# Kernel tuning notes

Measured on AMD Instinct MI355X. Metric: run time of the kernel, lower is better.

The kernel has to match this reference:

```python
import jax, jax.numpy as jnp
import numpy as np

N = 100000   # nodes
E = 1600000  # edges
DIM = 64
DIMS = [128, 64, 64, 64]  # [2*DIM] + 3*[DIM]
MAX_DEG = 64
NUM_LAB = 16

def _leaky(x):
    return jnp.where(x >= 0, x, 0.01 * x)

def _bn(x, g, b, eps=1e-5):
    # BatchNorm1d in training mode: per-feature batch mean / biased variance
    m = x.mean(axis=0)
    v = x.var(axis=0)
    return (x - m) * jax.lax.rsqrt(v + eps) * g + b

def setup_inputs() -> dict:
    key = jax.random.key(0)
    ks = jax.random.split(key, 40)
    d = {}
    d["node_deg"] = jax.random.randint(ks[0], (N,), 0, MAX_DEG + 1)
    d["node_lab"] = jax.random.randint(ks[1], (N,), 0, NUM_LAB)
    d["edge_index"] = jax.random.randint(ks[2], (2, E), 0, N)
    d["emb_deg"] = jax.random.normal(ks[3], (MAX_DEG + 1, DIM), jnp.float32) * 0.1
    d["emb_lab"] = jax.random.normal(ks[4], (NUM_LAB, DIM), jnp.float32) * 0.1
    k = 5
    for i, (n1, n2) in enumerate(zip(DIMS[:-1], DIMS[1:])):
        d[f"w{i}"] = jax.random.normal(ks[k], (n2, n1), jnp.float32) / np.sqrt(n1); k += 1
        d[f"b{i}"] = jnp.zeros((n2,), jnp.float32)
        d[f"g{i}"] = jnp.ones((n2,), jnp.float32)
        d[f"be{i}"] = jnp.zeros((n2,), jnp.float32)
    SUMD = sum(DIMS)  # 320
    d["fw1"] = jax.random.normal(ks[k], (DIM, SUMD), jnp.float32) / np.sqrt(SUMD); k += 1
    d["fb1"] = jnp.zeros((DIM,), jnp.float32)
    d["fg"] = jnp.ones((DIM,), jnp.float32)
    d["fbe"] = jnp.zeros((DIM,), jnp.float32)
    d["fw2"] = jax.random.normal(ks[k], (1, DIM), jnp.float32) / np.sqrt(DIM)
    d["fb2"] = jnp.zeros((1,), jnp.float32)
    return d

def reference(node_deg, node_lab, edge_index, emb_deg, emb_lab,
              w0, b0, g0, be0, w1, b1, g1, be1, w2, b2, g2, be2,
              fw1, fb1, fg, fbe, fw2, fb2):
    src, dst = edge_index[0], edge_index[1]
    # input embedding: concat of degree and label embeddings -> [N, 128]
    x0 = jnp.concatenate([emb_deg[node_deg], emb_lab[node_lab]], axis=1)
    z = [x0]
    for (w, b, g, be) in [(w0, b0, g0, be0), (w1, b1, g1, be1), (w2, b2, g2, be2)]:
        x = z[-1]
        # GINConv (eps=0): h = Linear(x + sum_{j in N(i)} x_j)
        agg = jax.ops.segment_sum(x[src], dst, num_segments=N)
        h = (x + agg) @ w.T + b
        z.append(_leaky(_bn(h, g, be)))
    xc = jnp.concatenate(z, axis=1)  # [N, 320]
    h = _leaky(_bn(xc @ fw1.T + fb1, fg, fbe))
    return jax.nn.sigmoid(h @ fw2.T + fb2).squeeze()  # [N]
```

## Files before the change

kernel.cpp:

```cpp
#include <hip/hip_runtime.h>
#include <math.h>

typedef __bf16 bf16;
typedef __attribute__((ext_vector_type(8))) __bf16 bf16x8;
typedef __attribute__((ext_vector_type(4))) float f32x4;

#define NBLK 128
#define NB_MAX 1600

__global__ __launch_bounds__(256) void embed_kernel(
    const int* __restrict__ deg, const int* __restrict__ lab,
    const float* __restrict__ ed, const float* __restrict__ el,
    bf16* __restrict__ x0, int n) {
  int idx = blockIdx.x * 256 + threadIdx.x;
  if (idx >= n * 16) return;
  int node = idx >> 4, q = idx & 15;
  const float* srcp = (q < 8) ? (ed + (size_t)deg[node] * 64 + q * 8)
                              : (el + (size_t)lab[node] * 64 + (q - 8) * 8);
  float4 a = ((const float4*)srcp)[0];
  float4 b = ((const float4*)srcp)[1];
  union { bf16 h[8]; uint4 u; } out;
  out.h[0] = (bf16)a.x; out.h[1] = (bf16)a.y; out.h[2] = (bf16)a.z; out.h[3] = (bf16)a.w;
  out.h[4] = (bf16)b.x; out.h[5] = (bf16)b.y; out.h[6] = (bf16)b.z; out.h[7] = (bf16)b.w;
  *(uint4*)(x0 + (size_t)idx * 8) = out.u;
}

__global__ __launch_bounds__(256) void bin_hist_kernel(const int* __restrict__ dst,
                                                       int* __restrict__ cnt,
                                                       int E, int ch, int nb) {
  __shared__ int lcnt[NB_MAX];
  int tid = threadIdx.x, blk = blockIdx.x;
  for (int t = tid; t < nb; t += 256) lcnt[t] = 0;
  __syncthreads();
  int base = blk * ch, eend = min(E, base + ch);
  for (int e = base + tid; e < eend; e += 256) atomicAdd(&lcnt[dst[e] >> 6], 1);
  __syncthreads();
  for (int t = tid; t < nb; t += 256) cnt[blk * nb + t] = lcnt[t];
}

__global__ __launch_bounds__(256) void bin_tot_kernel(const int* __restrict__ cnt,
                                                      int* __restrict__ tot, int nb) {
  int b = blockIdx.x * 256 + threadIdx.x;
  if (b >= nb) return;
  int s = 0;
  for (int blk = 0; blk < NBLK; ++blk) s += cnt[blk * nb + b];
  tot[b] = s;
}

__global__ __launch_bounds__(256) void scan_buckets_kernel(const int* __restrict__ tot,
                                                           int* __restrict__ bucketptr, int nb) {
  __shared__ int lds[256];
  int tid = threadIdx.x;
  const int CH = 7;
  int vals[CH];
  int s = 0;
#pragma unroll
  for (int k = 0; k < CH; ++k) {
    int i = tid * CH + k;
    vals[k] = (i < nb) ? tot[i] : 0;
    s += vals[k];
  }
  lds[tid] = s;
  __syncthreads();
  for (int off = 1; off < 256; off <<= 1) {
    int v = (tid >= off) ? lds[tid - off] : 0;
    __syncthreads();
    lds[tid] += v;
    __syncthreads();
  }
  int run = lds[tid] - s;
  if (tid == 0) bucketptr[0] = 0;
#pragma unroll
  for (int k = 0; k < CH; ++k) {
    int i = tid * CH + k;
    run += vals[k];
    if (i < nb) bucketptr[i + 1] = run;
  }
}

__global__ __launch_bounds__(256) void bin_off_kernel(const int* __restrict__ cnt,
                                                      const int* __restrict__ bucketptr,
                                                      int* __restrict__ woff, int nb) {
  int b = blockIdx.x * 256 + threadIdx.x;
  if (b >= nb) return;
  int run = bucketptr[b];
  for (int blk = 0; blk < NBLK; ++blk) {
    woff[blk * nb + b] = run;
    run += cnt[blk * nb + b];
  }
}

__global__ __launch_bounds__(256) void bin_scatter_kernel(const int* __restrict__ src,
                                                          const int* __restrict__ dst,
                                                          const int* __restrict__ woff,
                                                          int* __restrict__ packed,
                                                          int E, int ch, int nb) {
  __shared__ int cur[NB_MAX];
  int tid = threadIdx.x, blk = blockIdx.x;
  for (int t = tid; t < nb; t += 256) cur[t] = woff[blk * nb + t];
  __syncthreads();
  int base = blk * ch, eend = min(E, base + ch);
  for (int e = base + tid; e < eend; e += 256) {
    int d = dst[e], s = src[e];
    int pos = atomicAdd(&cur[d >> 6], 1);
    packed[pos] = ((d & 63) << 17) | s;
  }
}

__global__ __launch_bounds__(256) void csr_finalize_kernel(
    const int* __restrict__ packed, const int* __restrict__ bucketptr,
    int* __restrict__ rowptr, int* __restrict__ colidx, int n, int E) {
  __shared__ int hist[64], offs[64];
  int tid = threadIdx.x, b = blockIdx.x;
  if (tid < 64) hist[tid] = 0;
  __syncthreads();
  int beg = bucketptr[b], end = bucketptr[b + 1];
  for (int e = beg + tid; e < end; e += 256) atomicAdd(&hist[packed[e] >> 17], 1);
  __syncthreads();
  if (tid == 0) {
    int run = 0;
    for (int j = 0; j < 64; ++j) { offs[j] = run; run += hist[j]; }
  }
  __syncthreads();
  if (tid < 64) {
    int idx = b * 64 + tid;
    if (idx < n) rowptr[idx] = beg + offs[tid];
    hist[tid] = offs[tid];
  }
  if (b == 0 && tid == 64) rowptr[n] = E;
  __syncthreads();
  for (int e = beg + tid; e < end; e += 256) {
    int w = packed[e];
    int pos = atomicAdd(&hist[w >> 17], 1);
    colidx[beg + pos] = w & 0x1FFFF;
  }
}

__global__ __launch_bounds__(256) void mfma_gemm0(
    const bf16* __restrict__ x, const float* __restrict__ W,
    bf16* __restrict__ y, int n) {
  __shared__ bf16 As[64][136];
  __shared__ bf16 Bs[64][136];
  int tid = threadIdx.x;
  int nbase = blockIdx.x * 64;
  {
    int r = tid >> 2, c = tid & 3;
    int node = nbase + r;
    uint4 v[4] = {};
    if (node < n) {
      const uint4* p = (const uint4*)(x + (size_t)node * 128 + c * 32);
#pragma unroll
      for (int j = 0; j < 4; ++j) v[j] = p[j];
    }
#pragma unroll
    for (int j = 0; j < 4; ++j) *(uint4*)&As[r][c * 32 + j * 8] = v[j];
    const float4* wp = (const float4*)(W + r * 128 + c * 32);
#pragma unroll
    for (int j = 0; j < 4; ++j) {
      float4 f0 = wp[j * 2], f1 = wp[j * 2 + 1];
      union { bf16 h[8]; uint4 u; } t;
      t.h[0] = (bf16)f0.x; t.h[1] = (bf16)f0.y; t.h[2] = (bf16)f0.z; t.h[3] = (bf16)f0.w;
      t.h[4] = (bf16)f1.x; t.h[5] = (bf16)f1.y; t.h[6] = (bf16)f1.z; t.h[7] = (bf16)f1.w;
      *(uint4*)&Bs[r][c * 32 + j * 8] = t.u;
    }
  }
  __syncthreads();
  int l = tid & 63, w = tid >> 6, m = l & 15, quad = l >> 4;
  f32x4 acc[4] = {{0.f, 0.f, 0.f, 0.f}, {0.f, 0.f, 0.f, 0.f},
                  {0.f, 0.f, 0.f, 0.f}, {0.f, 0.f, 0.f, 0.f}};
#pragma unroll
  for (int k0 = 0; k0 < 128; k0 += 32) {
    bf16x8 a = *(const bf16x8*)&As[w * 16 + m][k0 + quad * 8];
#pragma unroll
    for (int t = 0; t < 4; ++t) {
      bf16x8 b = *(const bf16x8*)&Bs[t * 16 + m][k0 + quad * 8];
      acc[t] = __builtin_amdgcn_mfma_f32_16x16x32_bf16(a, b, acc[t], 0, 0, 0);
    }
  }
#pragma unroll
  for (int t = 0; t < 4; ++t)
#pragma unroll
    for (int r4 = 0; r4 < 4; ++r4) {
      int node = nbase + w * 16 + quad * 4 + r4;
      if (node < n) y[(size_t)node * 64 + t * 16 + m] = (bf16)acc[t][r4];
    }
}

__global__ __launch_bounds__(256) void mfma_gemm_bn(
    const bf16* __restrict__ hin, const float* __restrict__ st,
    const float* __restrict__ W, bf16* __restrict__ z,
    bf16* __restrict__ y, int n) {
  __shared__ bf16 As[64][72];
  __shared__ bf16 Bs[64][72];
  int tid = threadIdx.x;
  int nbase = blockIdx.x * 64;
  {
    int r = tid >> 2, c = tid & 3;
    int node = nbase + r;
    union { bf16 h[16]; uint4 u[2]; } t;
    if (node < n) {
      const uint4* p = (const uint4*)(hin + (size_t)node * 64 + c * 16);
      union { uint4 u; bf16 h[8]; } a0, a1;
      a0.u = p[0]; a1.u = p[1];
#pragma unroll
      for (int j = 0; j < 8; ++j) {
        int d = c * 16 + j;
        float v = (float)a0.h[j] * st[128 + d] + st[192 + d];
        v = (v >= 0.f) ? v : 0.01f * v;
        t.h[j] = (bf16)v;
      }
#pragma unroll
      for (int j = 0; j < 8; ++j) {
        int d = c * 16 + 8 + j;
        float v = (float)a1.h[j] * st[128 + d] + st[192 + d];
        v = (v >= 0.f) ? v : 0.01f * v;
        t.h[8 + j] = (bf16)v;
      }
      *(uint4*)(z + (size_t)node * 64 + c * 16) = t.u[0];
      *(uint4*)(z + (size_t)node * 64 + c * 16 + 8) = t.u[1];
    } else {
      t.u[0] = uint4{0, 0, 0, 0}; t.u[1] = uint4{0, 0, 0, 0};
    }
    *(uint4*)&As[r][c * 16] = t.u[0];
    *(uint4*)&As[r][c * 16 + 8] = t.u[1];
    const float4* wp = (const float4*)(W + r * 64 + c * 16);
#pragma unroll
    for (int j = 0; j < 2; ++j) {
      float4 f0 = wp[j * 2], f1 = wp[j * 2 + 1];
      union { bf16 h[8]; uint4 u; } tw;
      tw.h[0] = (bf16)f0.x; tw.h[1] = (bf16)f0.y; tw.h[2] = (bf16)f0.z; tw.h[3] = (bf16)f0.w;
      tw.h[4] = (bf16)f1.x; tw.h[5] = (bf16)f1.y; tw.h[6] = (bf16)f1.z; tw.h[7] = (bf16)f1.w;
      *(uint4*)&Bs[r][c * 16 + j * 8] = tw.u;
    }
  }
  __syncthreads();
  int l = tid & 63, w = tid >> 6, m = l & 15, quad = l >> 4;
  f32x4 acc[4] = {{0.f, 0.f, 0.f, 0.f}, {0.f, 0.f, 0.f, 0.f},
                  {0.f, 0.f, 0.f, 0.f}, {0.f, 0.f, 0.f, 0.f}};
#pragma unroll
  for (int k0 = 0; k0 < 64; k0 += 32) {
    bf16x8 a = *(const bf16x8*)&As[w * 16 + m][k0 + quad * 8];
#pragma unroll
    for (int t = 0; t < 4; ++t) {
      bf16x8 b = *(const bf16x8*)&Bs[t * 16 + m][k0 + quad * 8];
      acc[t] = __builtin_amdgcn_mfma_f32_16x16x32_bf16(a, b, acc[t], 0, 0, 0);
    }
  }
#pragma unroll
  for (int t = 0; t < 4; ++t)
#pragma unroll
    for (int r4 = 0; r4 < 4; ++r4) {
      int node = nbase + w * 16 + quad * 4 + r4;
      if (node < n) y[(size_t)node * 64 + t * 16 + m] = (bf16)acc[t][r4];
    }
}

__global__ __launch_bounds__(256) void gather_kernel(
    const bf16* __restrict__ y, const int* __restrict__ rowptr,
    const int* __restrict__ colidx, const float* __restrict__ bias,
    bf16* __restrict__ h, float* __restrict__ stats, int n) {
  __shared__ float s_sum[64], s_sq[64];
  int tid = threadIdx.x;
  if (tid < 64) { s_sum[tid] = 0.f; s_sq[tid] = 0.f; }
  __syncthreads();
  int lane = tid & 63, wv = tid >> 6;
  float bv = bias[lane];
  float psum = 0.f, psq = 0.f;
  int stride = gridDim.x * 8;
  const bf16* yl = y + lane;
  for (int nodeA = blockIdx.x * 8 + wv * 2; nodeA < n; nodeA += stride) {
    int nodeB = nodeA + 1;
    bool hasB = nodeB < n;
    float acc0 = (float)yl[(size_t)nodeA * 64] + bv;
    float acc1 = hasB ? (float)yl[(size_t)nodeB * 64] + bv : 0.f;
    int e0 = rowptr[nodeA], f0 = rowptr[nodeA + 1];
    int e1 = hasB ? rowptr[nodeB] : 0;
    int f1 = hasB ? rowptr[nodeB + 1] : 0;
    while (e0 + 8 <= f0 && e1 + 8 <= f1) {
      int a0 = colidx[e0], a1 = colidx[e0 + 1], a2 = colidx[e0 + 2], a3 = colidx[e0 + 3];
      int a4 = colidx[e0 + 4], a5 = colidx[e0 + 5], a6 = colidx[e0 + 6], a7 = colidx[e0 + 7];
      int b0 = colidx[e1], b1 = colidx[e1 + 1], b2 = colidx[e1 + 2], b3 = colidx[e1 + 3];
      int b4 = colidx[e1 + 4], b5 = colidx[e1 + 5], b6 = colidx[e1 + 6], b7 = colidx[e1 + 7];
      float va0 = (float)yl[(size_t)a0 * 64], va1 = (float)yl[(size_t)a1 * 64];
      float va2 = (float)yl[(size_t)a2 * 64], va3 = (float)yl[(size_t)a3 * 64];
      float va4 = (float)yl[(size_t)a4 * 64], va5 = (float)yl[(size_t)a5 * 64];
      float va6 = (float)yl[(size_t)a6 * 64], va7 = (float)yl[(size_t)a7 * 64];
      float vb0 = (float)yl[(size_t)b0 * 64], vb1 = (float)yl[(size_t)b1 * 64];
      float vb2 = (float)yl[(size_t)b2 * 64], vb3 = (float)yl[(size_t)b3 * 64];
      float vb4 = (float)yl[(size_t)b4 * 64], vb5 = (float)yl[(size_t)b5 * 64];
      float vb6 = (float)yl[(size_t)b6 * 64], vb7 = (float)yl[(size_t)b7 * 64];
      acc0 += ((va0 + va1) + (va2 + va3)) + ((va4 + va5) + (va6 + va7));
      acc1 += ((vb0 + vb1) + (vb2 + vb3)) + ((vb4 + vb5) + (vb6 + vb7));
      e0 += 8; e1 += 8;
    }
    for (; e0 + 4 <= f0; e0 += 4) {
      int a0 = colidx[e0], a1 = colidx[e0 + 1], a2 = colidx[e0 + 2], a3 = colidx[e0 + 3];
      float v0 = (float)yl[(size_t)a0 * 64], v1 = (float)yl[(size_t)a1 * 64];
      float v2 = (float)yl[(size_t)a2 * 64], v3 = (float)yl[(size_t)a3 * 64];
      acc0 += (v0 + v1) + (v2 + v3);
    }
    for (; e0 < f0; ++e0) acc0 += (float)yl[(size_t)colidx[e0] * 64];
    for (; e1 + 4 <= f1; e1 += 4) {
      int b0 = colidx[e1], b1 = colidx[e1 + 1], b2 = colidx[e1 + 2], b3 = colidx[e1 + 3];
      float v0 = (float)yl[(size_t)b0 * 64], v1 = (float)yl[(size_t)b1 * 64];
      float v2 = (float)yl[(size_t)b2 * 64], v3 = (float)yl[(size_t)b3 * 64];
      acc1 += (v0 + v1) + (v2 + v3);
    }
    for (; e1 < f1; ++e1) acc1 += (float)yl[(size_t)colidx[e1] * 64];
    h[(size_t)nodeA * 64 + lane] = (bf16)acc0;
    psum += acc0; psq += acc0 * acc0;
    if (hasB) {
      h[(size_t)nodeB * 64 + lane] = (bf16)acc1;
      psum += acc1; psq += acc1 * acc1;
    }
  }
  atomicAdd(&s_sum[lane], psum);
  atomicAdd(&s_sq[lane], psq);
  __syncthreads();
  if (tid < 64) {
    atomicAdd(&stats[tid], s_sum[tid]);
    atomicAdd(&stats[64 + tid], s_sq[tid]);
  }
}

__global__ __launch_bounds__(256) void mfma_final(
    const bf16* __restrict__ x0, const bf16* __restrict__ z1,
    const bf16* __restrict__ z2, const bf16* __restrict__ h2,
    const float* __restrict__ st2, const float* __restrict__ fw1,
    const float* __restrict__ fb1, bf16* __restrict__ hf,
    float* __restrict__ stats, int n) {
  __shared__ bf16 As[64][136];
  __shared__ bf16 Bs[64][136];
  __shared__ float s_sum[64], s_sq[64];
  int tid = threadIdx.x;
  if (tid < 64) { s_sum[tid] = 0.f; s_sq[tid] = 0.f; }
  int nbase = blockIdx.x * 64;
  int l = tid & 63, w = tid >> 6, m = l & 15, quad = l >> 4;
  int r = tid >> 2, c = tid & 3;
  int node_r = nbase + r;
  f32x4 acc[4] = {{0.f, 0.f, 0.f, 0.f}, {0.f, 0.f, 0.f, 0.f},
                  {0.f, 0.f, 0.f, 0.f}, {0.f, 0.f, 0.f, 0.f}};

#pragma unroll
  for (int seg = 0; seg < 4; ++seg) {
    __syncthreads();
    if (seg == 0) {
      uint4 v[4] = {};
      if (node_r < n) {
        const uint4* p = (const uint4*)(x0 + (size_t)node_r * 128 + c * 32);
#pragma unroll
        for (int j = 0; j < 4; ++j) v[j] = p[j];
      }
#pragma unroll
      for (int j = 0; j < 4; ++j) *(uint4*)&As[r][c * 32 + j * 8] = v[j];
      const float4* wp = (const float4*)(fw1 + r * 320 + c * 32);
#pragma unroll
      for (int j = 0; j < 4; ++j) {
        float4 f0 = wp[j * 2], f1 = wp[j * 2 + 1];
        union { bf16 h[8]; uint4 u; } t;
        t.h[0] = (bf16)f0.x; t.h[1] = (bf16)f0.y; t.h[2] = (bf16)f0.z; t.h[3] = (bf16)f0.w;
        t.h[4] = (bf16)f1.x; t.h[5] = (bf16)f1.y; t.h[6] = (bf16)f1.z; t.h[7] = (bf16)f1.w;
        *(uint4*)&Bs[r][c * 32 + j * 8] = t.u;
      }
    } else if (seg < 3) {
      const bf16* zz = (seg == 1) ? z1 : z2;
      uint4 v[2] = {};
      if (node_r < n) {
        const uint4* p = (const uint4*)(zz + (size_t)node_r * 64 + c * 16);
        v[0] = p[0]; v[1] = p[1];
      }
      *(uint4*)&As[r][c * 16] = v[0];
      *(uint4*)&As[r][c * 16 + 8] = v[1];
      const float4* wp = (const float4*)(fw1 + r * 320 + (seg == 1 ? 128 : 192) + c * 16);
#pragma unroll
      for (int j = 0; j < 2; ++j) {
        float4 f0 = wp[j * 2], f1 = wp[j * 2 + 1];
        union { bf16 h[8]; uint4 u; } t;
        t.h[0] = (bf16)f0.x; t.h[1] = (bf16)f0.y; t.h[2] = (bf16)f0.z; t.h[3] = (bf16)f0.w;
        t.h[4] = (bf16)f1.x; t.h[5] = (bf16)f1.y; t.h[6] = (bf16)f1.z; t.h[7] = (bf16)f1.w;
        *(uint4*)&Bs[r][c * 16 + j * 8] = t.u;
      }
    } else {
      union { bf16 h[16]; uint4 u[2]; } t;
      if (node_r < n) {
        const uint4* p = (const uint4*)(h2 + (size_t)node_r * 64 + c * 16);
        union { uint4 u; bf16 h[8]; } a0, a1;
        a0.u = p[0]; a1.u = p[1];
#pragma unroll
        for (int j = 0; j < 8; ++j) {
          int d = c * 16 + j;
          float v = (float)a0.h[j] * st2[128 + d] + st2[192 + d];
          v = (v >= 0.f) ? v : 0.01f * v;
          t.h[j] = (bf16)v;
        }
#pragma unroll
        for (int j = 0; j < 8; ++j) {
          int d = c * 16 + 8 + j;
          float v = (float)a1.h[j] * st2[128 + d] + st2[192 + d];
          v = (v >= 0.f) ? v : 0.01f * v;
          t.h[8 + j] = (bf16)v;
        }
      } else {
        t.u[0] = uint4{0, 0, 0, 0}; t.u[1] = uint4{0, 0, 0, 0};
      }
      *(uint4*)&As[r][c * 16] = t.u[0];
      *(uint4*)&As[r][c * 16 + 8] = t.u[1];
      const float4* wp = (const float4*)(fw1 + r * 320 + 256 + c * 16);
#pragma unroll
      for (int j = 0; j < 2; ++j) {
        float4 f0 = wp[j * 2], f1 = wp[j * 2 + 1];
        union { bf16 h[8]; uint4 u; } tw;
        tw.h[0] = (bf16)f0.x; tw.h[1] = (bf16)f0.y; tw.h[2] = (bf16)f0.z; tw.h[3] = (bf16)f0.w;
        tw.h[4] = (bf16)f1.x; tw.h[5] = (bf16)f1.y; tw.h[6] = (bf16)f1.z; tw.h[7] = (bf16)f1.w;
        *(uint4*)&Bs[r][c * 16 + j * 8] = tw.u;
      }
    }
    __syncthreads();
    int kmax = (seg == 0) ? 128 : 64;
    for (int k0 = 0; k0 < kmax; k0 += 32) {
      bf16x8 a = *(const bf16x8*)&As[w * 16 + m][k0 + quad * 8];
#pragma unroll
      for (int t = 0; t < 4; ++t) {
        bf16x8 b = *(const bf16x8*)&Bs[t * 16 + m][k0 + quad * 8];
        acc[t] = __builtin_amdgcn_mfma_f32_16x16x32_bf16(a, b, acc[t], 0, 0, 0);
      }
    }
  }

#pragma unroll
  for (int t = 0; t < 4; ++t) {
    int o = t * 16 + m;
    float bv = fb1[o];
    float s = 0.f, q = 0.f;
#pragma unroll
    for (int r4 = 0; r4 < 4; ++r4) {
      int node = nbase + w * 16 + quad * 4 + r4;
      if (node < n) {
        float v = acc[t][r4] + bv;
        hf[(size_t)node * 64 + o] = (bf16)v;
        s += v;
        q += v * v;
      }
    }
    atomicAdd(&s_sum[o], s);
    atomicAdd(&s_sq[o], q);
  }
  __syncthreads();
  if (tid < 64) {
    atomicAdd(&stats[tid], s_sum[tid]);
    atomicAdd(&stats[64 + tid], s_sq[tid]);
  }
}

__global__ void bn_finalize_kernel(float* __restrict__ st, const float* __restrict__ g,
                                   const float* __restrict__ be, float inv_n) {
  int o = threadIdx.x;
  if (o < 64) {
    float mean = st[o] * inv_n;
    float var = st[64 + o] * inv_n - mean * mean;
    float sc = g[o] * rsqrtf(var + 1e-5f);
    st[128 + o] = sc;
    st[192 + o] = be[o] - mean * sc;
  }
}

__global__ __launch_bounds__(256) void final_out_kernel(const bf16* __restrict__ hf,
                                                        const float* __restrict__ st,
                                                        const float* __restrict__ fw2,
                                                        const float* __restrict__ fb2,
                                                        float* __restrict__ out, int n) {
  int lane = threadIdx.x & 63;
  int node = blockIdx.x * 4 + (threadIdx.x >> 6);
  if (node >= n) return;
  float v = (float)hf[(size_t)node * 64 + lane] * st[128 + lane] + st[192 + lane];
  v = (v >= 0.f) ? v : 0.01f * v;
  v *= fw2[lane];
#pragma unroll
  for (int off = 32; off > 0; off >>= 1) v += __shfl_xor(v, off);
  if (lane == 0) out[node] = 1.f / (1.f + expf(-(v + fb2[0])));
}

extern "C" void kernel_launch(void* const* d_in, const int* in_sizes, int n_in,
                              void* d_out, int out_size, void* d_ws, size_t ws_size,
                              hipStream_t stream) {
  const int* node_deg = (const int*)d_in[0];
  const int* node_lab = (const int*)d_in[1];
  const int* ei = (const int*)d_in[2];
  const float* emb_deg = (const float*)d_in[3];
  const float* emb_lab = (const float*)d_in[4];
  const float* w0 = (const float*)d_in[5];
  const float* b0 = (const float*)d_in[6];
  const float* g0 = (const float*)d_in[7];
  const float* be0 = (const float*)d_in[8];
  const float* w1 = (const float*)d_in[9];
  const float* b1 = (const float*)d_in[10];
  const float* g1 = (const float*)d_in[11];
  const float* be1 = (const float*)d_in[12];
  const float* w2 = (const float*)d_in[13];
  const float* b2 = (const float*)d_in[14];
  const float* g2 = (const float*)d_in[15];
  const float* be2 = (const float*)d_in[16];
  const float* fw1 = (const float*)d_in[17];
  const float* fb1 = (const float*)d_in[18];
  const float* fg = (const float*)d_in[19];
  const float* fbe = (const float*)d_in[20];
  const float* fw2 = (const float*)d_in[21];
  const float* fb2 = (const float*)d_in[22];

  const int N = in_sizes[0];
  const int E = in_sizes[2] / 2;
  const int* src = ei;
  const int* dst = ei + E;
  const int NB = (N + 63) >> 6;
  const int CH = (E + NBLK - 1) / NBLK;

  char* ws = (char*)d_ws;
  size_t off = 0;
  auto alloc = [&](size_t bytes) {
    void* p = ws + off;
    off += (bytes + 255) & ~(size_t)255;
    return p;
  };
  bf16* x0 = (bf16*)alloc((size_t)N * 128 * 2);
  bf16* z1 = (bf16*)alloc((size_t)N * 64 * 2);
  bf16* z2 = (bf16*)alloc((size_t)N * 64 * 2);
  bf16* h = (bf16*)alloc((size_t)N * 64 * 2);
  bf16* y = (bf16*)alloc((size_t)N * 64 * 2);
  int* packed = (int*)alloc((size_t)E * 4);
  int* colidx = (int*)alloc((size_t)E * 4);
  int* rowptr = (int*)alloc((size_t)(N + 1) * 4);
  int* cnt = (int*)alloc((size_t)NBLK * NB * 4);
  int* woff = (int*)alloc((size_t)NBLK * NB * 4);
  int* btot = (int*)alloc((size_t)NB * 4);
  int* bucketptr = (int*)alloc((size_t)(NB + 1) * 4);
  float* stats = (float*)alloc(4 * 256 * 4);

  hipMemsetAsync(stats, 0, 4 * 256 * 4, stream);

  embed_kernel<<<(N * 16 + 255) / 256, 256, 0, stream>>>(node_deg, node_lab, emb_deg,
                                                         emb_lab, x0, N);
  bin_hist_kernel<<<NBLK, 256, 0, stream>>>(dst, cnt, E, CH, NB);
  bin_tot_kernel<<<(NB + 255) / 256, 256, 0, stream>>>(cnt, btot, NB);
  scan_buckets_kernel<<<1, 256, 0, stream>>>(btot, bucketptr, NB);
  bin_off_kernel<<<(NB + 255) / 256, 256, 0, stream>>>(cnt, bucketptr, woff, NB);
  bin_scatter_kernel<<<NBLK, 256, 0, stream>>>(src, dst, woff, packed, E, CH, NB);
  csr_finalize_kernel<<<NB, 256, 0, stream>>>(packed, bucketptr, rowptr, colidx, N, E);

  int ngrid = (N + 63) / 64;
  int ggrid = 2048;

  mfma_gemm0<<<ngrid, 256, 0, stream>>>(x0, w0, y, N);
  gather_kernel<<<ggrid, 256, 0, stream>>>(y, rowptr, colidx, b0, h, stats, N);
  bn_finalize_kernel<<<1, 64, 0, stream>>>(stats, g0, be0, 1.0f / N);
  mfma_gemm_bn<<<ngrid, 256, 0, stream>>>(h, stats, w1, z1, y, N);
  gather_kernel<<<ggrid, 256, 0, stream>>>(y, rowptr, colidx, b1, h, stats + 256, N);
  bn_finalize_kernel<<<1, 64, 0, stream>>>(stats + 256, g1, be1, 1.0f / N);
  mfma_gemm_bn<<<ngrid, 256, 0, stream>>>(h, stats + 256, w2, z2, y, N);
  gather_kernel<<<ggrid, 256, 0, stream>>>(y, rowptr, colidx, b2, h, stats + 512, N);
  bn_finalize_kernel<<<1, 64, 0, stream>>>(stats + 512, g2, be2, 1.0f / N);
  mfma_final<<<ngrid, 256, 0, stream>>>(x0, z1, z2, h, stats + 512, fw1, fb1, y,
                                        stats + 768, N);
  bn_finalize_kernel<<<1, 64, 0, stream>>>(stats + 768, fg, fbe, 1.0f / N);
  final_out_kernel<<<(N + 3) / 4, 256, 0, stream>>>(y, stats + 768, fw2, fb2,
                                                    (float*)d_out, N);
}
```

Before: 622.9 us.

## Vectorize neighbor gather per node and fold BN finalize into consumer kernels

New measurement: 670.8 us. +7.7%, slower.

```diff
diff --git a/kernel.cpp b/kernel.cpp
--- a/kernel.cpp
+++ b/kernel.cpp
@@ -7,6 +7,15 @@
 
 #define NBLK 128
 #define NB_MAX 1600
+
+__device__ __forceinline__ void bn_coeffs(const float* st, const float* g,
+                                          const float* be, float inv_n, int d,
+                                          float& sc, float& sh) {
+  float mean = st[d] * inv_n;
+  float var = st[64 + d] * inv_n - mean * mean;
+  sc = g[d] * rsqrtf(var + 1e-5f);
+  sh = be[d] - mean * sc;
+}
 
 __global__ __launch_bounds__(256) void embed_kernel(
     const int* __restrict__ deg, const int* __restrict__ lab,
@@ -188,12 +197,20 @@
 
 __global__ __launch_bounds__(256) void mfma_gemm_bn(
     const bf16* __restrict__ hin, const float* __restrict__ st,
+    const float* __restrict__ g, const float* __restrict__ be, float inv_n,
     const float* __restrict__ W, bf16* __restrict__ z,
     bf16* __restrict__ y, int n) {
   __shared__ bf16 As[64][72];
   __shared__ bf16 Bs[64][72];
+  __shared__ float ssc[64], ssh[64];
   int tid = threadIdx.x;
   int nbase = blockIdx.x * 64;
+  if (tid < 64) {
+    float sc, sh;
+    bn_coeffs(st, g, be, inv_n, tid, sc, sh);
+    ssc[tid] = sc; ssh[tid] = sh;
+  }
+  __syncthreads();
   {
     int r = tid >> 2, c = tid & 3;
     int node = nbase + r;
@@ -205,14 +222,14 @@
 #pragma unroll
       for (int j = 0; j < 8; ++j) {
         int d = c * 16 + j;
-        float v = (float)a0.h[j] * st[128 + d] + st[192 + d];
+        float v = (float)a0.h[j] * ssc[d] + ssh[d];
         v = (v >= 0.f) ? v : 0.01f * v;
         t.h[j] = (bf16)v;
       }
 #pragma unroll
       for (int j = 0; j < 8; ++j) {
         int d = c * 16 + 8 + j;
-        float v = (float)a1.h[j] * st[128 + d] + st[192 + d];
+        float v = (float)a1.h[j] * ssc[d] + ssh[d];
         v = (v >= 0.f) ? v : 0.01f * v;
         t.h[8 + j] = (bf16)v;
       }
@@ -264,58 +281,56 @@
   if (tid < 64) { s_sum[tid] = 0.f; s_sq[tid] = 0.f; }
   __syncthreads();
   int lane = tid & 63, wv = tid >> 6;
-  float bv = bias[lane];
-  float psum = 0.f, psq = 0.f;
-  int stride = gridDim.x * 8;
-  const bf16* yl = y + lane;
-  for (int nodeA = blockIdx.x * 8 + wv * 2; nodeA < n; nodeA += stride) {
-    int nodeB = nodeA + 1;
-    bool hasB = nodeB < n;
-    float acc0 = (float)yl[(size_t)nodeA * 64] + bv;
-    float acc1 = hasB ? (float)yl[(size_t)nodeB * 64] + bv : 0.f;
-    int e0 = rowptr[nodeA], f0 = rowptr[nodeA + 1];
-    int e1 = hasB ? rowptr[nodeB] : 0;
-    int f1 = hasB ? rowptr[nodeB + 1] : 0;
-    while (e0 + 8 <= f0 && e1 + 8 <= f1) {
-      int a0 = colidx[e0], a1 = colidx[e0 + 1], a2 = colidx[e0 + 2], a3 = colidx[e0 + 3];
-      int a4 = colidx[e0 + 4], a5 = colidx[e0 + 5], a6 = colidx[e0 + 6], a7 = colidx[e0 + 7];
-      int b0 = colidx[e1], b1 = colidx[e1 + 1], b2 = colidx[e1 + 2], b3 = colidx[e1 + 3];
-      int b4 = colidx[e1 + 4], b5 = colidx[e1 + 5], b6 = colidx[e1 + 6], b7 = colidx[e1 + 7];
-      float va0 = (float)yl[(size_t)a0 * 64], va1 = (float)yl[(size_t)a1 * 64];
-      float va2 = (float)yl[(size_t)a2 * 64], va3 = (float)yl[(size_t)a3 * 64];
-      float va4 = (float)yl[(size_t)a4 * 64], va5 = (float)yl[(size_t)a5 * 64];
-      float va6 = (float)yl[(size_t)a6 * 64], va7 = (float)yl[(size_t)a7 * 64];
-      float vb0 = (float)yl[(size_t)b0 * 64], vb1 = (float)yl[(size_t)b1 * 64];
-      float vb2 = (float)yl[(size_t)b2 * 64], vb3 = (float)yl[(size_t)b3 * 64];
-      float vb4 = (float)yl[(size_t)b4 * 64], vb5 = (float)yl[(size_t)b5 * 64];
-      float vb6 = (float)yl[(size_t)b6 * 64], vb7 = (float)yl[(size_t)b7 * 64];
-      acc0 += ((va0 + va1) + (va2 + va3)) + ((va4 + va5) + (va6 + va7));
-      acc1 += ((vb0 + vb1) + (vb2 + vb3)) + ((vb4 + vb5) + (vb6 + vb7));
-      e0 += 8; e1 += 8;
-    }
-    for (; e0 + 4 <= f0; e0 += 4) {
-      int a0 = colidx[e0], a1 = colidx[e0 + 1], a2 = colidx[e0 + 2], a3 = colidx[e0 + 3];
-      float v0 = (float)yl[(size_t)a0 * 64], v1 = (float)yl[(size_t)a1 * 64];
-      float v2 = (float)yl[(size_t)a2 * 64], v3 = (float)yl[(size_t)a3 * 64];
-      acc0 += (v0 + v1) + (v2 + v3);
-    }
-    for (; e0 < f0; ++e0) acc0 += (float)yl[(size_t)colidx[e0] * 64];
-    for (; e1 + 4 <= f1; e1 += 4) {
-      int b0 = colidx[e1], b1 = colidx[e1 + 1], b2 = colidx[e1 + 2], b3 = colidx[e1 + 3];
-      float v0 = (float)yl[(size_t)b0 * 64], v1 = (float)yl[(size_t)b1 * 64];
-      float v2 = (float)yl[(size_t)b2 * 64], v3 = (float)yl[(size_t)b3 * 64];
-      acc1 += (v0 + v1) + (v2 + v3);
-    }
-    for (; e1 < f1; ++e1) acc1 += (float)yl[(size_t)colidx[e1] * 64];
-    h[(size_t)nodeA * 64 + lane] = (bf16)acc0;
-    psum += acc0; psq += acc0 * acc0;
-    if (hasB) {
-      h[(size_t)nodeB * 64 + lane] = (bf16)acc1;
-      psum += acc1; psq += acc1 * acc1;
-    }
-  }
-  atomicAdd(&s_sum[lane], psum);
-  atomicAdd(&s_sq[lane], psq);
+  int g = lane >> 4;
+  int lq = lane & 15;
+  float4 bv = *(const float4*)(bias + lq * 4);
+  float p0 = 0, p1 = 0, p2 = 0, p3 = 0, q0 = 0, q1 = 0, q2 = 0, q3 = 0;
+  int stride = gridDim.x * 4;
+  for (int node = blockIdx.x * 4 + wv; node < n; node += stride) {
+    int beg = rowptr[node], end = rowptr[node + 1];
+    float a0 = 0, a1 = 0, a2 = 0, a3 = 0;
+    for (int e = beg; e < end; e += 16) {
+#pragma unroll
+      for (int b = 0; b < 4; ++b) {
+        int ee = e + b * 4 + g;
+        bool valid = ee < end;
+        int src = colidx[valid ? ee : (end - 1)];
+        uint2 d = *(const uint2*)(y + (size_t)src * 64 + lq * 4);
+        if (!valid) { d.x = 0u; d.y = 0u; }
+        union { unsigned u; float f; } f0, f1, f2, f3;
+        f0.u = d.x << 16; f1.u = d.x & 0xFFFF0000u;
+        f2.u = d.y << 16; f3.u = d.y & 0xFFFF0000u;
+        a0 += f0.f; a1 += f1.f; a2 += f2.f; a3 += f3.f;
+      }
+    }
+    a0 += __shfl_xor(a0, 16); a1 += __shfl_xor(a1, 16);
+    a2 += __shfl_xor(a2, 16); a3 += __shfl_xor(a3, 16);
+    a0 += __shfl_xor(a0, 32); a1 += __shfl_xor(a1, 32);
+    a2 += __shfl_xor(a2, 32); a3 += __shfl_xor(a3, 32);
+    uint2 sd = *(const uint2*)(y + (size_t)node * 64 + lq * 4);
+    union { unsigned u; float f; } s0, s1, s2, s3;
+    s0.u = sd.x << 16; s1.u = sd.x & 0xFFFF0000u;
+    s2.u = sd.y << 16; s3.u = sd.y & 0xFFFF0000u;
+    float v0 = a0 + s0.f + bv.x;
+    float v1 = a1 + s1.f + bv.y;
+    float v2 = a2 + s2.f + bv.z;
+    float v3 = a3 + s3.f + bv.w;
+    if (g == 0) {
+      union { bf16 hh[4]; uint2 u; } o;
+      o.hh[0] = (bf16)v0; o.hh[1] = (bf16)v1; o.hh[2] = (bf16)v2; o.hh[3] = (bf16)v3;
+      *(uint2*)(h + (size_t)node * 64 + lq * 4) = o.u;
+      p0 += v0; q0 += v0 * v0;
+      p1 += v1; q1 += v1 * v1;
+      p2 += v2; q2 += v2 * v2;
+      p3 += v3; q3 += v3 * v3;
+    }
+  }
+  if (g == 0) {
+    atomicAdd(&s_sum[lq * 4 + 0], p0); atomicAdd(&s_sq[lq * 4 + 0], q0);
+    atomicAdd(&s_sum[lq * 4 + 1], p1); atomicAdd(&s_sq[lq * 4 + 1], q1);
+    atomicAdd(&s_sum[lq * 4 + 2], p2); atomicAdd(&s_sq[lq * 4 + 2], q2);
+    atomicAdd(&s_sum[lq * 4 + 3], p3); atomicAdd(&s_sq[lq * 4 + 3], q3);
+  }
   __syncthreads();
   if (tid < 64) {
     atomicAdd(&stats[tid], s_sum[tid]);
@@ -326,14 +341,20 @@
 __global__ __launch_bounds__(256) void mfma_final(
     const bf16* __restrict__ x0, const bf16* __restrict__ z1,
     const bf16* __restrict__ z2, const bf16* __restrict__ h2,
-    const float* __restrict__ st2, const float* __restrict__ fw1,
-    const float* __restrict__ fb1, bf16* __restrict__ hf,
-    float* __restrict__ stats, int n) {
+    const float* __restrict__ st2, const float* __restrict__ g2,
+    const float* __restrict__ be2, float inv_n,
+    const float* __restrict__ fw1, const float* __restrict__ fb1,
+    bf16* __restrict__ hf, float* __restrict__ stats, int n) {
   __shared__ bf16 As[64][136];
   __shared__ bf16 Bs[64][136];
-  __shared__ float s_sum[64], s_sq[64];
+  __shared__ float s_sum[64], s_sq[64], ssc[64], ssh[64];
   int tid = threadIdx.x;
-  if (tid < 64) { s_sum[tid] = 0.f; s_sq[tid] = 0.f; }
+  if (tid < 64) {
+    s_sum[tid] = 0.f; s_sq[tid] = 0.f;
+    float sc, sh;
+    bn_coeffs(st2, g2, be2, inv_n, tid, sc, sh);
+    ssc[tid] = sc; ssh[tid] = sh;
+  }
   int nbase = blockIdx.x * 64;
   int l = tid & 63, w = tid >> 6, m = l & 15, quad = l >> 4;
   int r = tid >> 2, c = tid & 3;
@@ -389,14 +410,14 @@
 #pragma unroll
         for (int j = 0; j < 8; ++j) {
           int d = c * 16 + j;
-          float v = (float)a0.h[j] * st2[128 + d] + st2[192 + d];
+          float v = (float)a0.h[j] * ssc[d] + ssh[d];
           v = (v >= 0.f) ? v : 0.01f * v;
           t.h[j] = (bf16)v;
         }
 #pragma unroll
         for (int j = 0; j < 8; ++j) {
           int d = c * 16 + 8 + j;
-          float v = (float)a1.h[j] * st2[128 + d] + st2[192 + d];
+          float v = (float)a1.h[j] * ssc[d] + ssh[d];
           v = (v >= 0.f) ? v : 0.01f * v;
           t.h[8 + j] = (bf16)v;
         }
@@ -452,27 +473,17 @@
   }
 }
 
-__global__ void bn_finalize_kernel(float* __restrict__ st, const float* __restrict__ g,
-                                   const float* __restrict__ be, float inv_n) {
-  int o = threadIdx.x;
-  if (o < 64) {
-    float mean = st[o] * inv_n;
-    float var = st[64 + o] * inv_n - mean * mean;
-    float sc = g[o] * rsqrtf(var + 1e-5f);
-    st[128 + o] = sc;
-    st[192 + o] = be[o] - mean * sc;
-  }
-}
-
-__global__ __launch_bounds__(256) void final_out_kernel(const bf16* __restrict__ hf,
-                                                        const float* __restrict__ st,
-                                                        const float* __restrict__ fw2,
-                                                        const float* __restrict__ fb2,
-                                                        float* __restrict__ out, int n) {
+__global__ __launch_bounds__(256) void final_out_kernel(
+    const bf16* __restrict__ hf, const float* __restrict__ st,
+    const float* __restrict__ g, const float* __restrict__ be, float inv_n,
+    const float* __restrict__ fw2, const float* __restrict__ fb2,
+    float* __restrict__ out, int n) {
   int lane = threadIdx.x & 63;
   int node = blockIdx.x * 4 + (threadIdx.x >> 6);
   if (node >= n) return;
-  float v = (float)hf[(size_t)node * 64 + lane] * st[128 + lane] + st[192 + lane];
+  float sc, sh;
+  bn_coeffs(st, g, be, inv_n, lane, sc, sh);
+  float v = (float)hf[(size_t)node * 64 + lane] * sc + sh;
   v = (v >= 0.f) ? v : 0.01f * v;
   v *= fw2[lane];
 #pragma unroll
@@ -513,6 +524,7 @@
   const int* dst = ei + E;
   const int NB = (N + 63) >> 6;
   const int CH = (E + NBLK - 1) / NBLK;
+  const float inv_n = 1.0f / N;
 
   char* ws = (char*)d_ws;
   size_t off = 0;
@@ -547,20 +559,16 @@
   csr_finalize_kernel<<<NB, 256, 0, stream>>>(packed, bucketptr, rowptr, colidx, N, E);
 
   int ngrid = (N + 63) / 64;
-  int ggrid = 2048;
+  int ggrid = 4096;
 
   mfma_gemm0<<<ngrid, 256, 0, stream>>>(x0, w0, y, N);
   gather_kernel<<<ggrid, 256, 0, stream>>>(y, rowptr, colidx, b0, h, stats, N);
-  bn_finalize_kernel<<<1, 64, 0, stream>>>(stats, g0, be0, 1.0f / N);
-  mfma_gemm_bn<<<ngrid, 256, 0, stream>>>(h, stats, w1, z1, y, N);
+  mfma_gemm_bn<<<ngrid, 256, 0, stream>>>(h, stats, g0, be0, inv_n, w1, z1, y, N);
   gather_kernel<<<ggrid, 256, 0, stream>>>(y, rowptr, colidx, b1, h, stats + 256, N);
-  bn_finalize_kernel<<<1, 64, 0, stream>>>(stats + 256, g1, be1, 1.0f / N);
-  mfma_gemm_bn<<<ngrid, 256, 0, stream>>>(h, stats + 256, w2, z2, y, N);
+  mfma_gemm_bn<<<ngrid, 256, 0, stream>>>(h, stats + 256, g1, be1, inv_n, w2, z2, y, N);
   gather_kernel<<<ggrid, 256, 0, stream>>>(y, rowptr, colidx, b2, h, stats + 512, N);
-  bn_finalize_kernel<<<1, 64, 0, stream>>>(stats + 512, g2, be2, 1.0f / N);
-  mfma_final<<<ngrid, 256, 0, stream>>>(x0, z1, z2, h, stats + 512, fw1, fb1, y,
-                                        stats + 768, N);
-  bn_finalize_kernel<<<1, 64, 0, stream>>>(stats + 768, fg, fbe, 1.0f / N);
-  final_out_kernel<<<(N + 3) / 4, 256, 0, stream>>>(y, stats + 768, fw2, fb2,
-                                                    (float*)d_out, N);
-}
+  mfma_final<<<ngrid, 256, 0, stream>>>(x0, z1, z2, h, stats + 512, g2, be2, inv_n,
+                                        fw1, fb1, y, stats + 768, N);
+  final_out_kernel<<<(N + 3) / 4, 256, 0, stream>>>(y, stats + 768, fg, fbe, inv_n,
+                                                    fw2, fb2, (float*)d_out, N);
+}
```
